# Performance work log

Hardware: AMD Instinct MI355X
Metric: run time of the kernel (lower is better)

The kernel has to match this reference:

```python
import jax, jax.numpy as jnp
import numpy as np

VOXEL_SIZE = 96
SHARPNESS = 100.0
EPS = 1e-8


def _grid_coords(V):
    # matches torch: x fastest, normalized by (V-1); shape [V*V, 2] as (x, y)
    y, x = jnp.meshgrid(jnp.arange(V, dtype=jnp.float32), jnp.arange(V, dtype=jnp.float32), indexing='ij')
    return jnp.stack([x.ravel(), y.ravel()], axis=1) / float(V - 1)


def setup_inputs() -> dict:
    key = jax.random.key(0)
    k1, k2, k3 = jax.random.split(key, 3)
    B, N, P = 4, 32, 32
    polygons = jax.random.uniform(k1, (B, N, P, 2), dtype=jnp.float32)
    attributes = jax.random.uniform(k2, (B, 8), dtype=jnp.float32)
    validity_scores = jax.random.uniform(k3, (B, N), dtype=jnp.float32)
    return {"polygons": polygons, "attributes": attributes, "validity_scores": validity_scores}


def _polygon_masks(polygons, coords):
    # polygons: [B,N,P,2], coords: [M,2] -> soft occupancy masks [B,N,M]
    v0 = polygons                              # [B,N,P,2]
    v1 = jnp.roll(polygons, -1, axis=2)        # next vertex (closed loop)
    e = v1 - v0                                # edges [B,N,P,2]
    pts = coords[None, None, None]             # [1,1,1,M,2]
    v = pts - v0[:, :, :, None, :]             # [B,N,P,M,2]
    e_sq = (e * e).sum(-1) + EPS               # [B,N,P]
    t = (v * e[:, :, :, None, :]).sum(-1) / e_sq[..., None]   # [B,N,P,M]
    t = jnp.clip(t, 0.0, 1.0)
    proj = v0[:, :, :, None, :] + t[..., None] * e[:, :, :, None, :]
    diff = pts - proj
    dists = jnp.sqrt((diff * diff).sum(-1))    # [B,N,P,M]
    min_dist = dists.min(axis=2)               # [B,N,M] min over edges
    # ray-casting point-in-polygon (horizontal ray toward +x)
    x_pts = coords[:, 0]                        # [M]
    y_pts = coords[:, 1]
    x0, y0 = v0[..., 0:1], v0[..., 1:2]        # [B,N,P,1]
    x1, y1 = v1[..., 0:1], v1[..., 1:2]
    y_crosses = ((y0 <= y_pts) & (y1 > y_pts)) | ((y1 <= y_pts) & (y0 > y_pts))
    inter_x = x0 + (x1 - x0) * ((y_pts - y0) / (y1 - y0 + EPS))
    crossings = (inter_x > x_pts) & y_crosses  # [B,N,P,M]
    inside = (crossings.sum(axis=2) % 2) == 1  # [B,N,M]
    sdf = jnp.where(inside, -min_dist, min_dist)
    return jax.nn.sigmoid(-sdf * SHARPNESS)    # [B,N,M]


def reference(polygons, attributes, validity_scores):
    B = polygons.shape[0]
    V = VOXEL_SIZE
    coords = _grid_coords(V)                                   # [V*V, 2]
    masks = _polygon_masks(polygons, coords)                   # [B,N,M]
    valid = validity_scores >= 0.5                             # [B,N]
    combined = jnp.max(jnp.where(valid[:, :, None], masks, 0.0), axis=1)  # [B,M]
    combined = combined.reshape(B, V, V)                       # [B,H,W]
    # height extrusion: int(round(clamp(attr,0,1)*D)), clamped to [1,D]; non-differentiable
    norm_h = jnp.clip(attributes[:, 0], 0.0, 1.0)
    hv = jnp.clip(jnp.round(norm_h * V), 1.0, float(V))        # [B]
    hv = jax.lax.stop_gradient(hv)
    depth_mask = (jnp.arange(V, dtype=jnp.float32)[None, :] < hv[:, None]).astype(combined.dtype)  # [B,D]
    voxels = combined[:, None, :, :] * depth_mask[:, :, None, None]  # [B,D,H,W]
    return voxels
```

## Files before the change

kernel.cpp:

```cpp
#include <hip/hip_runtime.h>

#define V 96
#define VV (V * V)
#define V3 (V * V * V)
#define B_ 4
#define N_ 32
#define P_ 32
#define NE (N_ * P_)
#define TILE 64
#define TPB 512
#define NW (TPB / 64)
#define TILES_PER_B (VV / TILE)

__global__ __launch_bounds__(TPB) void fused_kernel(
    const float* __restrict__ poly,
    const float* __restrict__ attr,
    const float* __restrict__ validity,
    float4* __restrict__ out)
{
    __shared__ float4 se0[NE];
    __shared__ float4 se1[NE];
    __shared__ float2 sraw[NE];
    __shared__ float  spart[NW][TILE];
    __shared__ __align__(16) float sfinal[TILE];
    __shared__ int svalidIdx[N_];
    __shared__ int scnt;

    const int b       = blockIdx.x / TILES_PER_B;
    const int tileInB = blockIdx.x - b * TILES_PER_B;
    const int pix0    = tileInB * TILE;
    const int tid     = threadIdx.x;
    const int s       = tid >> 6;
    const int lane    = tid & 63;

    {
        const float4* pg = (const float4*)(poly + (size_t)b * (NE * 2));
        ((float4*)sraw)[tid] = pg[tid];
    }
    if (tid < 64) {
        bool v = (tid < N_) && (validity[b * N_ + tid] >= 0.5f);
        unsigned long long m = __ballot(v);
        if (v) svalidIdx[__popcll(m & ((1ull << tid) - 1))] = tid;
        if (tid == 0) scnt = (int)__popcll(m);
    }
    __syncthreads();

    #pragma unroll
    for (int i = 0; i < 2; ++i) {
        int e  = tid + i * TPB;
        int p  = e & (P_ - 1);
        int en = (e & ~(P_ - 1)) | ((p + 1) & (P_ - 1));
        float2 v0 = sraw[e];
        float2 v1 = sraw[en];
        float ex = v1.x - v0.x, ey = v1.y - v0.y;
        se0[e] = make_float4(v0.x, v0.y, ex, ey);
        se1[e] = make_float4(__builtin_amdgcn_rcpf(ex * ex + ey * ey + 1e-8f),
                             __builtin_amdgcn_rcpf(ey + 1e-8f),
                             v1.y,
                             0.0f);
    }
    __syncthreads();

    const int pixel = pix0 + lane;
    const int py_i  = pixel / V;
    const int px_i  = pixel - py_i * V;
    const float px = (float)px_i / 95.0f;
    const float py = (float)py_i / 95.0f;

    const int cnt = scnt;
    float pmax = 0.0f;

    for (int j = s; j < cnt; j += NW) {
        const int base = svalidIdx[j] << 5;
        float mind2 = 1e30f;
        int par = 0;
        #pragma unroll 8
        for (int p = 0; p < P_; ++p) {
            float4 e0 = se0[base + p];
            float4 e1 = se1[base + p];
            float vx = px - e0.x, vy = py - e0.y;
            float t  = (vx * e0.z + vy * e0.w) * e1.x;
            t = fminf(fmaxf(t, 0.0f), 1.0f);
            float dx = vx - t * e0.z, dy = vy - t * e0.w;
            mind2 = fminf(mind2, dx * dx + dy * dy);
            bool c0 = (e0.y <= py);
            bool c1 = (e1.z <= py);
            float ix = e0.x + e0.z * (vy * e1.y);
            par ^= (int)((c0 != c1) & (ix > px));
        }
        float mind = sqrtf(mind2);
        float sdf  = par ? -mind : mind;
        float m = 1.0f / (1.0f + __expf(sdf * 100.0f));
        pmax = fmaxf(pmax, m);
    }

    spart[s][lane] = pmax;
    __syncthreads();
    if (tid < 64) {
        float f = spart[0][lane];
        #pragma unroll
        for (int w = 1; w < NW; ++w) f = fmaxf(f, spart[w][lane]);
        sfinal[lane] = f;
    }
    __syncthreads();

    float a  = attr[b * 8];
    float nh = fminf(fmaxf(a, 0.0f), 1.0f);
    float hv = fminf(fmaxf(rintf(nh * (float)V), 1.0f), (float)V);
    int hvi = (int)hv;

    const float4* sf4 = (const float4*)sfinal;
    size_t obase = (size_t)b * (V3 / 4) + (size_t)(pix0 >> 2);
    #pragma unroll
    for (int k = 0; k < 3; ++k) {
        int idx = k * TPB + tid;
        int d   = idx >> 4;
        int x4  = idx & 15;
        float4 val = sf4[x4];
        float keep = (d < hvi) ? 1.0f : 0.0f;
        out[obase + (size_t)d * (VV / 4) + x4] =
            make_float4(val.x * keep, val.y * keep, val.z * keep, val.w * keep);
    }
}

extern "C" void kernel_launch(void* const* d_in, const int* in_sizes, int n_in,
                              void* d_out, int out_size, void* d_ws, size_t ws_size,
                              hipStream_t stream) {
    const float* polygons = (const float*)d_in[0];
    const float* attrs    = (const float*)d_in[1];
    const float* validity = (const float*)d_in[2];
    float4* out = (float4*)d_out;

    fused_kernel<<<B_ * TILES_PER_B, TPB, 0, stream>>>(polygons, attrs, validity, out);
}
```

Before: 74.31 us.

## Precompute edge data in separate kernel and read via scalar loads

Edge setup (vertices, edge vectors, reciprocals) moves into a separate small kernel that writes to workspace. The main kernel then reads each polygon's edges from global memory with wave-uniform addresses, so they can be served by scalar loads instead of LDS staging, and drops the per-block staging and its barrier. The main kernel also doubles the block size to 1024 threads, computes ray-cast parity with ballots instead of per-lane XOR, and uses fmed3 for the clamp. The trade-offs are an extra kernel launch, a dependency on the workspace buffer, and reliance on scalar-cache hits for the edge data.

```diff
diff --git a/kernel.cpp b/kernel.cpp
--- a/kernel.cpp
+++ b/kernel.cpp
@@ -8,20 +8,34 @@
 #define P_ 32
 #define NE (N_ * P_)
 #define TILE 64
-#define TPB 512
+#define TPB 1024
 #define NW (TPB / 64)
 #define TILES_PER_B (VV / TILE)
 
-__global__ __launch_bounds__(TPB) void fused_kernel(
+__global__ __launch_bounds__(256) void edge_kernel(
     const float* __restrict__ poly,
+    float4* __restrict__ es)
+{
+    const int e = blockIdx.x * 256 + threadIdx.x;
+    const float2* p2 = (const float2*)poly;
+    const int en = (e & ~(P_ - 1)) | ((e + 1) & (P_ - 1));
+    float2 v0 = p2[e];
+    float2 v1 = p2[en];
+    float ex = v1.x - v0.x, ey = v1.y - v0.y;
+    es[e * 2]     = make_float4(v0.x, v0.y, ex, ey);
+    es[e * 2 + 1] = make_float4(__builtin_amdgcn_rcpf(ex * ex + ey * ey + 1e-8f),
+                                __builtin_amdgcn_rcpf(ey + 1e-8f),
+                                v1.y,
+                                0.0f);
+}
+
+__global__ __launch_bounds__(TPB, 8) void fused_kernel(
+    const float* __restrict__ es,
     const float* __restrict__ attr,
     const float* __restrict__ validity,
     float4* __restrict__ out)
 {
-    __shared__ float4 se0[NE];
-    __shared__ float4 se1[NE];
-    __shared__ float2 sraw[NE];
-    __shared__ float  spart[NW][TILE];
+    __shared__ float spart[NW][TILE];
     __shared__ __align__(16) float sfinal[TILE];
     __shared__ int svalidIdx[N_];
     __shared__ int scnt;
@@ -33,31 +47,11 @@
     const int s       = tid >> 6;
     const int lane    = tid & 63;
 
-    {
-        const float4* pg = (const float4*)(poly + (size_t)b * (NE * 2));
-        ((float4*)sraw)[tid] = pg[tid];
-    }
     if (tid < 64) {
         bool v = (tid < N_) && (validity[b * N_ + tid] >= 0.5f);
         unsigned long long m = __ballot(v);
         if (v) svalidIdx[__popcll(m & ((1ull << tid) - 1))] = tid;
         if (tid == 0) scnt = (int)__popcll(m);
-    }
-    __syncthreads();
-
-    #pragma unroll
-    for (int i = 0; i < 2; ++i) {
-        int e  = tid + i * TPB;
-        int p  = e & (P_ - 1);
-        int en = (e & ~(P_ - 1)) | ((p + 1) & (P_ - 1));
-        float2 v0 = sraw[e];
-        float2 v1 = sraw[en];
-        float ex = v1.x - v0.x, ey = v1.y - v0.y;
-        se0[e] = make_float4(v0.x, v0.y, ex, ey);
-        se1[e] = make_float4(__builtin_amdgcn_rcpf(ex * ex + ey * ey + 1e-8f),
-                             __builtin_amdgcn_rcpf(ey + 1e-8f),
-                             v1.y,
-                             0.0f);
     }
     __syncthreads();
 
@@ -71,25 +65,33 @@
     float pmax = 0.0f;
 
     for (int j = s; j < cnt; j += NW) {
-        const int base = svalidIdx[j] << 5;
+        const int nidx = __builtin_amdgcn_readfirstlane(svalidIdx[j]);
+        const float* E = es + ((size_t)(b * N_ + nidx) << 8);
+
         float mind2 = 1e30f;
-        int par = 0;
-        #pragma unroll 8
+        unsigned long long pm = 0ull;
+        bool cprev = (E[1] <= py);
+
+        #pragma unroll 4
         for (int p = 0; p < P_; ++p) {
-            float4 e0 = se0[base + p];
-            float4 e1 = se1[base + p];
-            float vx = px - e0.x, vy = py - e0.y;
-            float t  = (vx * e0.z + vy * e0.w) * e1.x;
-            t = fminf(fmaxf(t, 0.0f), 1.0f);
-            float dx = vx - t * e0.z, dy = vy - t * e0.w;
+            const float* e8 = E + (p << 3);
+            float x0 = e8[0], y0 = e8[1];
+            float ex = e8[2], ey = e8[3];
+            float rq = e8[4], ry = e8[5];
+            float y1 = e8[6];
+            float vx = px - x0, vy = py - y0;
+            float t  = (vx * ex + vy * ey) * rq;
+            t = __builtin_amdgcn_fmed3f(t, 0.0f, 1.0f);
+            float dx = vx - t * ex, dy = vy - t * ey;
             mind2 = fminf(mind2, dx * dx + dy * dy);
-            bool c0 = (e0.y <= py);
-            bool c1 = (e1.z <= py);
-            float ix = e0.x + e0.z * (vy * e1.y);
-            par ^= (int)((c0 != c1) & (ix > px));
+            bool cnext = (y1 <= py);
+            float ix = x0 + ex * (vy * ry);
+            pm ^= (__ballot(cprev != cnext) & __ballot(ix > px));
+            cprev = cnext;
         }
         float mind = sqrtf(mind2);
-        float sdf  = par ? -mind : mind;
+        bool inside = (pm >> lane) & 1ull;
+        float sdf  = inside ? -mind : mind;
         float m = 1.0f / (1.0f + __expf(sdf * 100.0f));
         pmax = fmaxf(pmax, m);
     }
@@ -112,14 +114,16 @@
     const float4* sf4 = (const float4*)sfinal;
     size_t obase = (size_t)b * (V3 / 4) + (size_t)(pix0 >> 2);
     #pragma unroll
-    for (int k = 0; k < 3; ++k) {
-        int idx = k * TPB + tid;
-        int d   = idx >> 4;
-        int x4  = idx & 15;
-        float4 val = sf4[x4];
-        float keep = (d < hvi) ? 1.0f : 0.0f;
-        out[obase + (size_t)d * (VV / 4) + x4] =
-            make_float4(val.x * keep, val.y * keep, val.z * keep, val.w * keep);
+    for (int k = 0; k < 2; ++k) {
+        int idx = tid + k * TPB;
+        if (idx < 1536) {
+            int d  = idx >> 4;
+            int x4 = idx & 15;
+            float4 val = sf4[x4];
+            float keep = (d < hvi) ? 1.0f : 0.0f;
+            out[obase + (size_t)d * (VV / 4) + x4] =
+                make_float4(val.x * keep, val.y * keep, val.z * keep, val.w * keep);
+        }
     }
 }
 
@@ -130,6 +134,8 @@
     const float* attrs    = (const float*)d_in[1];
     const float* validity = (const float*)d_in[2];
     float4* out = (float4*)d_out;
+    float* es   = (float*)d_ws;
 
-    fused_kernel<<<B_ * TILES_PER_B, TPB, 0, stream>>>(polygons, attrs, validity, out);
+    edge_kernel<<<(B_ * NE) / 256, 256, 0, stream>>>(polygons, (float4*)es);
+    fused_kernel<<<B_ * TILES_PER_B, TPB, 0, stream>>>(es, attrs, validity, out);
 }
```

New measurement: 75.56 us. About the same (+1.7%).
